# Kernel optimization log

Hardware: AMD Instinct MI355X
Metric: run time of the kernel (lower is better)

The kernel has to match this reference:

```python
import jax, jax.numpy as jnp
import numpy as np

DIM = 768
NUM_HEADS = 12
DIM_HEAD = 64
INNER = NUM_HEADS * DIM_HEAD  # 768
SCALE = DIM_HEAD ** -0.5


def setup_inputs() -> dict:
    key = jax.random.key(0)
    k1, k2, k3 = jax.random.split(key, 3)
    B, N = 8, 1024
    x = jax.random.normal(k1, (B, N, DIM), dtype=jnp.float32)
    # Linear(dim, 3*inner_dim, bias=False): weight shape (out, in) torch-style
    w_qkv = jax.random.normal(k2, (3 * INNER, DIM), dtype=jnp.float32) * (DIM ** -0.5)
    # proj: Linear(inner_dim, dim, bias=False)
    w_proj = jax.random.normal(k3, (DIM, INNER), dtype=jnp.float32) * (INNER ** -0.5)
    return {"x": x, "w_qkv": w_qkv, "w_proj": w_proj}


def reference(x, w_qkv, w_proj):
    B, N, C = x.shape
    H, dh = NUM_HEADS, DIM_HEAD
    # qkv projection: (B,N,C) @ (C, 3*inner) -> (B,N,3*inner)
    qkv = jnp.einsum('bnc,oc->bno', x, w_qkv)
    qkv = qkv.reshape(B, N, 3, H, dh).transpose(2, 0, 3, 1, 4)  # (3,B,H,N,dh)
    q, k, v = qkv[0], qkv[1], qkv[2]
    # attention scores (B,H,N,N)
    attn_scores = jnp.einsum('bhnd,bhmd->bhnm', q, k) * SCALE
    attn_probs = jax.nn.softmax(attn_scores, axis=-1)
    # attention output (B,H,N,dh) -> (B,N,inner)
    attn_out = jnp.einsum('bhnm,bhmd->bhnd', attn_probs, v)
    attn_out = attn_out.transpose(0, 2, 1, 3).reshape(B, N, H * dh)
    out = jnp.einsum('bni,oi->bno', attn_out, w_proj)
    return out
```

## Files before the change

kernel.cpp:

```cpp
#include <hip/hip_runtime.h>
#include <stdint.h>

typedef unsigned short u16;
typedef __attribute__((ext_vector_type(8))) short short8;
typedef __attribute__((ext_vector_type(4))) short short4v;
typedef __attribute__((ext_vector_type(4))) float f32x4;

#define LOG2E 1.44269504088896340736f

#define Bb 8
#define NSEQ 1024
#define DIMC 768
#define NH 12
#define DH 64
#define INNER 768
#define MTOT (Bb*NSEQ)
#define QKVN (3*INNER)
#define HEADS_TOT (Bb*NH)
#define QKV_PART ((size_t)Bb*NH*NSEQ*DH)

static __device__ inline u16 f2bf(float f) {
    uint32_t u = __builtin_bit_cast(uint32_t, f);
    uint32_t r = (u + 0x7fffu + ((u >> 16) & 1u)) >> 16;
    return (u16)r;
}

static __device__ __forceinline__ uint32_t pkbf(float f0, float f1) {
    uint32_t u0 = __builtin_bit_cast(uint32_t, f0) + 0x8000u;
    uint32_t u1 = __builtin_bit_cast(uint32_t, f1) + 0x8000u;
    return __builtin_amdgcn_perm(u1, u0, 0x07060302u);
}

#if __has_builtin(__builtin_amdgcn_mfma_f32_16x16x16bf16_1k)
static __device__ __forceinline__ f32x4 mfma16(short4v a, short4v b, f32x4 c) {
    return __builtin_amdgcn_mfma_f32_16x16x16bf16_1k(a, b, c, 0, 0, 0);
}
#else
static __device__ __forceinline__ f32x4 mfma16(short4v a, short4v b, f32x4 c) {
    asm volatile("v_mfma_f32_16x16x16_bf16 %0, %1, %2, %0\n\ts_nop 7\n\ts_nop 7"
                 : "+v"(c) : "v"(a), "v"(b));
    return c;
}
#endif

typedef __attribute__((address_space(1))) const void gas_void;
typedef __attribute__((address_space(3))) void las_void;
static __device__ __forceinline__ void async16(u16* lds, const u16* g) {
    __builtin_amdgcn_global_load_lds((gas_void*)(uintptr_t)g,
                                     (las_void*)(uintptr_t)lds, 16, 0, 0);
}

#define NX8  786432
#define NWQ8 221184
#define NWP8 73728
#define NCVT (NX8 + NWQ8 + NWP8)
__global__ __launch_bounds__(256) void cvt_all(const float* __restrict__ x,
                                               const float* __restrict__ wq,
                                               const float* __restrict__ wp,
                                               u16* __restrict__ xb,
                                               u16* __restrict__ wqb,
                                               u16* __restrict__ wpb) {
    int i = blockIdx.x * 256 + threadIdx.x;
    const float* s; u16* d; int j;
    if (i < NX8) { s = x; d = xb; j = i; }
    else if (i < NX8 + NWQ8) { s = wq; d = wqb; j = i - NX8; }
    else { s = wp; d = wpb; j = i - NX8 - NWQ8; }
    const float4* s4 = (const float4*)s;
    float4 a = s4[2 * j], b = s4[2 * j + 1];
    float v[8] = {a.x, a.y, a.z, a.w, b.x, b.y, b.z, b.w};
    u16 o[8];
#pragma unroll
    for (int t = 0; t < 8; t++) o[t] = f2bf(v[t]);
    ((uint4*)d)[j] = *(const uint4*)o;
}

#define BK 32
__global__ __launch_bounds__(512, 4) void gemm_qkv(const u16* __restrict__ A,
                                                   const u16* __restrict__ Bm,
                                                   u16* __restrict__ qkv) {
    __shared__ u16 As[128 * BK];
    __shared__ u16 Bs[256 * BK];
    const int tid = threadIdx.x;
    const int w = tid >> 6, lane = tid & 63, quad = lane >> 4, l16 = lane & 15;
    const int wr = w >> 2, wc = w & 3;
    const int m0 = blockIdx.y * 128;
    const int n0 = blockIdx.x * 256;
    const int K = DIMC;

    const int rl = lane >> 2, cc = lane & 3;
    const int ra = w * 16 + rl;
    const u16* agp = A + (size_t)(m0 + ra) * K + ((cc - ((ra >> 1) & 3)) & 3) * 8;
    u16* alp = As + (w * 16) * BK;
    const u16* bgp[2]; u16* blp[2];
#pragma unroll
    for (int j = 0; j < 2; j++) {
        int rb = w * 32 + j * 16 + rl;
        bgp[j] = Bm + (size_t)(n0 + rb) * K + ((cc - ((rb >> 1) & 3)) & 3) * 8;
        blp[j] = Bs + (w * 32 + j * 16) * BK;
    }

    const int swz = ((quad + ((l16 >> 1) & 3)) & 3) * 8;
    int aoff[4], boff[4];
#pragma unroll
    for (int t = 0; t < 4; t++) {
        aoff[t] = (wr * 64 + t * 16 + l16) * BK + swz;
        boff[t] = (wc * 64 + t * 16 + l16) * BK + swz;
    }

    f32x4 acc[4][4] = {};
    for (int kt = 0; kt < K; kt += BK) {
        __syncthreads();
        async16(alp, agp + kt);
        async16(blp[0], bgp[0] + kt);
        async16(blp[1], bgp[1] + kt);
        __syncthreads();
        short8 af[4], bf[4];
#pragma unroll
        for (int t = 0; t < 4; t++) af[t] = *(const short8*)(As + aoff[t]);
#pragma unroll
        for (int t = 0; t < 4; t++) bf[t] = *(const short8*)(Bs + boff[t]);
#pragma unroll
        for (int mt = 0; mt < 4; mt++)
#pragma unroll
            for (int nt = 0; nt < 4; nt++)
                acc[mt][nt] = __builtin_amdgcn_mfma_f32_16x16x32_bf16(af[mt], bf[nt],
                                                                      acc[mt][nt], 0, 0, 0);
    }

#pragma unroll
    for (int nt = 0; nt < 4; nt++) {
        int o = n0 + wc * 64 + nt * 16 + l16;
        int which = o / 768;
        int rem = o - which * 768;
        int h = rem >> 6, d = rem & 63;
        if (which == 2) {
            u16* vt = qkv + 2 * QKV_PART;
#pragma unroll
            for (int mt = 0; mt < 4; mt++) {
                int m = m0 + wr * 64 + mt * 16 + quad * 4;
                int bb = m >> 10, ns = m & 1023;
                alignas(8) u16 pk[4];
#pragma unroll
                for (int r = 0; r < 4; r++) pk[r] = f2bf(acc[mt][nt][r]);
                *(uint2*)(vt + ((size_t)(bb * NH + h) * DH + d) * NSEQ + ns) =
                    *(const uint2*)pk;
            }
        } else {
            float sc = (which == 0) ? (0.125f * LOG2E) : 1.0f;
#pragma unroll
            for (int mt = 0; mt < 4; mt++)
#pragma unroll
                for (int r = 0; r < 4; r++) {
                    int m = m0 + wr * 64 + mt * 16 + quad * 4 + r;
                    int bb = m >> 10, ns = m & 1023;
                    size_t idx = (size_t)which * QKV_PART +
                                 (((size_t)(bb * NH + h) * NSEQ + ns) << 6) + d;
                    qkv[idx] = f2bf(acc[mt][nt][r] * sc);
                }
        }
    }
}

__global__ __launch_bounds__(256) void gemm_proj(const u16* __restrict__ A,
                                                 const u16* __restrict__ Bm,
                                                 float* __restrict__ Co) {
    __shared__ u16 As[128 * BK];
    __shared__ u16 Bs[128 * BK];
    const int tid = threadIdx.x;
    const int w = tid >> 6, lane = tid & 63, quad = lane >> 4, l16 = lane & 15;
    const int wr = w >> 1, wc = w & 1;
    const int m0 = blockIdx.y * 128;
    const int n0 = blockIdx.x * 128;
    const int K = INNER, N = DIMC;

    const int rl = lane >> 2, cc = lane & 3;
    const u16* ag[2]; const u16* bg[2]; u16* al[2]; u16* bl[2];
#pragma unroll
    for (int j = 0; j < 2; j++) {
        int r = w * 32 + j * 16 + rl;
        int c = ((cc - ((r >> 1) & 3)) & 3) * 8;
        ag[j] = A + (size_t)(m0 + r) * K + c;
        bg[j] = Bm + (size_t)(n0 + r) * K + c;
        al[j] = As + (w * 32 + j * 16) * BK;
        bl[j] = Bs + (w * 32 + j * 16) * BK;
    }
    const int swz = ((quad + ((l16 >> 1) & 3)) & 3) * 8;
    int aoff[4], boff[4];
#pragma unroll
    for (int t = 0; t < 4; t++) {
        aoff[t] = (wr * 64 + t * 16 + l16) * BK + swz;
        boff[t] = (wc * 64 + t * 16 + l16) * BK + swz;
    }

    f32x4 acc[4][4] = {};
    for (int kt = 0; kt < K; kt += BK) {
        __syncthreads();
#pragma unroll
        for (int j = 0; j < 2; j++) {
            async16(al[j], ag[j] + kt);
            async16(bl[j], bg[j] + kt);
        }
        __syncthreads();
        short8 af[4], bf[4];
#pragma unroll
        for (int t = 0; t < 4; t++) af[t] = *(const short8*)(As + aoff[t]);
#pragma unroll
        for (int t = 0; t < 4; t++) bf[t] = *(const short8*)(Bs + boff[t]);
#pragma unroll
        for (int mt = 0; mt < 4; mt++)
#pragma unroll
            for (int nt = 0; nt < 4; nt++)
                acc[mt][nt] = __builtin_amdgcn_mfma_f32_16x16x32_bf16(af[mt], bf[nt],
                                                                      acc[mt][nt], 0, 0, 0);
    }
#pragma unroll
    for (int mt = 0; mt < 4; mt++)
#pragma unroll
        for (int nt = 0; nt < 4; nt++) {
            int o = n0 + wc * 64 + nt * 16 + l16;
#pragma unroll
            for (int r = 0; r < 4; r++) {
                int m = m0 + wr * 64 + mt * 16 + quad * 4 + r;
                Co[(size_t)m * N + o] = acc[mt][nt][r];
            }
        }
}

__global__ __launch_bounds__(256) void attn_kernel(const u16* __restrict__ qkv,
                                                   u16* __restrict__ attn) {
    __shared__ u16 Ks[64 * 64];
    __shared__ u16 Vs[64 * 64];

    const int tid = threadIdx.x;
    const int w = tid >> 6, lane = tid & 63, quad = lane >> 4, l16 = lane & 15;
    const int bh = blockIdx.y, qt = blockIdx.x;
    const size_t headoff = (size_t)bh * NSEQ * DH;
    const u16* Qp = qkv + headoff;
    const u16* Kp = qkv + QKV_PART + headoff;
    const u16* Vtp = qkv + 2 * QKV_PART + headoff;
    const int q0 = qt * 128 + w * 32;

    const int rl8 = lane >> 3, cc8 = lane & 7;
    const u16* kg[2]; const u16* vg[2]; u16* kl[2]; u16* vl[2];
#pragma unroll
    for (int j = 0; j < 2; j++) {
        int r = w * 16 + j * 8 + rl8;
        int c = ((cc8 - r) & 7) * 8;
        kg[j] = Kp + (size_t)r * DH + c;
        vg[j] = Vtp + (size_t)r * NSEQ + c;
        kl[j] = Ks + (w * 16 + j * 8) * 64;
        vl[j] = Vs + (w * 16 + j * 8) * 64;
    }

    const int sw0 = ((quad + l16) & 7) * 8;
    const int sw1 = ((quad + 4 + l16) & 7) * 8;

    short8 qf[2][2];
#pragma unroll
    for (int mf = 0; mf < 2; mf++) {
        qf[mf][0] = *(const short8*)(Qp + (size_t)(q0 + mf * 16 + l16) * DH + quad * 8);
        qf[mf][1] = *(const short8*)(Qp + (size_t)(q0 + mf * 16 + l16) * DH + 32 + quad * 8);
    }

    f32x4 oacc[2][4] = {};
    float lsum[2] = {0.f, 0.f};

    for (int kt = 0; kt < NSEQ; kt += 64) {
        __syncthreads();
#pragma unroll
        for (int j = 0; j < 2; j++) {
            async16(kl[j], kg[j] + (size_t)kt * DH);
            async16(vl[j], vg[j] + kt);
        }
        __syncthreads();

        short8 kf[4][2];
#pragma unroll
        for (int nt = 0; nt < 4; nt++) {
            const u16* kr = Ks + (nt * 16 + l16) * 64;
            kf[nt][0] = *(const short8*)(kr + sw0);
            kf[nt][1] = *(const short8*)(kr + sw1);
        }
        short4v vf[4][4];
#pragma unroll
        for (int nt2 = 0; nt2 < 4; nt2++) {
            int row = nt2 * 16 + l16;
#pragma unroll
            for (int c = 0; c < 4; c++) {
                int off = row * 64 + (((c * 2 + (quad >> 1) + row) & 7) << 3) + (quad & 1) * 4;
                vf[nt2][c] = *(const short4v*)(Vs + off);
            }
        }

#pragma unroll
        for (int mf = 0; mf < 2; mf++) {
            f32x4 st[4];
#pragma unroll
            for (int nt = 0; nt < 4; nt++) {
                f32x4 z = {};
                z = __builtin_amdgcn_mfma_f32_16x16x32_bf16(kf[nt][0], qf[mf][0], z, 0, 0, 0);
                z = __builtin_amdgcn_mfma_f32_16x16x32_bf16(kf[nt][1], qf[mf][1], z, 0, 0, 0);
                st[nt] = z;
            }
            short4v pf[4];
#pragma unroll
            for (int c = 0; c < 4; c++) {
                float p0 = __builtin_amdgcn_exp2f(st[c][0]);
                float p1 = __builtin_amdgcn_exp2f(st[c][1]);
                float p2 = __builtin_amdgcn_exp2f(st[c][2]);
                float p3 = __builtin_amdgcn_exp2f(st[c][3]);
                lsum[mf] += (p0 + p1) + (p2 + p3);
                uint2 u = {pkbf(p0, p1), pkbf(p2, p3)};
                pf[c] = __builtin_bit_cast(short4v, u);
            }
#pragma unroll
            for (int nt2 = 0; nt2 < 4; nt2++)
#pragma unroll
                for (int c = 0; c < 4; c++)
                    oacc[mf][nt2] = mfma16(vf[nt2][c], pf[c], oacc[mf][nt2]);
        }
    }

#pragma unroll
    for (int mf = 0; mf < 2; mf++) {
        float v = lsum[mf];
        v += __shfl_xor(v, 16);
        v += __shfl_xor(v, 32);
        lsum[mf] = 1.0f / v;
    }

    const int b = bh / NH, h = bh - (bh / NH) * NH;
#pragma unroll
    for (int mf = 0; mf < 2; mf++) {
        int q = q0 + mf * 16 + l16;
        float inv = lsum[mf];
#pragma unroll
        for (int nt2 = 0; nt2 < 4; nt2++) {
            uint2 u = {pkbf(oacc[mf][nt2][0] * inv, oacc[mf][nt2][1] * inv),
                       pkbf(oacc[mf][nt2][2] * inv, oacc[mf][nt2][3] * inv)};
            int d = nt2 * 16 + quad * 4;
            *(uint2*)(attn + ((size_t)(b * NSEQ + q)) * INNER + h * DH + d) = u;
        }
    }
}

extern "C" void kernel_launch(void* const* d_in, const int* in_sizes, int n_in,
                              void* d_out, int out_size, void* d_ws, size_t ws_size,
                              hipStream_t stream) {
    const float* x = (const float*)d_in[0];
    const float* w_qkv = (const float*)d_in[1];
    const float* w_proj = (const float*)d_in[2];
    float* out = (float*)d_out;

    u16* xb = (u16*)d_ws;
    u16* wqkvb = xb + 6291456;
    u16* wprojb = wqkvb + 1769472;
    u16* qkvb = wprojb + 589824;
    u16* attnb = qkvb + 18874368;

    cvt_all<<<NCVT / 256, 256, 0, stream>>>(x, w_qkv, w_proj, xb, wqkvb, wprojb);

    dim3 g1(QKVN / 256, MTOT / 128);
    gemm_qkv<<<g1, 512, 0, stream>>>(xb, wqkvb, qkvb);

    dim3 g2(NSEQ / 128, HEADS_TOT);
    attn_kernel<<<g2, 256, 0, stream>>>(qkvb, attnb);

    dim3 g3(INNER / 128, MTOT / 128);
    gemm_proj<<<g3, 256, 0, stream>>>(attnb, wprojb, out);
}
```

Baseline: 207.1 us.

## Double K-tile depth in GEMMs and attention, add XCD-aware block remapping

Both GEMMs move from a 32-wide to a 64-wide K tile with an 8-chunk XOR swizzle, which halves the number of barrier pairs per output tile. Attention now stages 128 keys per iteration instead of 64 and processes them in two halves. Block indices are remapped so that blocks sharing A rows land on the same XCD, and the attention grid is transposed so heads vary fastest. The intent is to cut synchronisation overhead and improve L2 locality, at the cost of double the shared memory per block, which may reduce occupancy.

```diff
diff --git a/kernel.cpp b/kernel.cpp
--- a/kernel.cpp
+++ b/kernel.cpp
@@ -74,7 +74,7 @@
     ((uint4*)d)[j] = *(const uint4*)o;
 }
 
-#define BK 32
+#define BK 64
 __global__ __launch_bounds__(512, 4) void gemm_qkv(const u16* __restrict__ A,
                                                    const u16* __restrict__ Bm,
                                                    u16* __restrict__ qkv) {
@@ -83,48 +83,59 @@
     const int tid = threadIdx.x;
     const int w = tid >> 6, lane = tid & 63, quad = lane >> 4, l16 = lane & 15;
     const int wr = w >> 2, wc = w & 3;
-    const int m0 = blockIdx.y * 128;
-    const int n0 = blockIdx.x * 256;
+    const int bid = blockIdx.x + 9 * blockIdx.y;
+    const int xcd = bid & 7, slot = bid >> 3;
+    const int m0 = (xcd + 8 * (slot / 9)) * 128;
+    const int n0 = (slot % 9) * 256;
     const int K = DIMC;
 
-    const int rl = lane >> 2, cc = lane & 3;
-    const int ra = w * 16 + rl;
-    const u16* agp = A + (size_t)(m0 + ra) * K + ((cc - ((ra >> 1) & 3)) & 3) * 8;
-    u16* alp = As + (w * 16) * BK;
-    const u16* bgp[2]; u16* blp[2];
+    const int rl8 = lane >> 3, cc8 = lane & 7;
+    const u16* agp[2]; int asl[2];
 #pragma unroll
     for (int j = 0; j < 2; j++) {
-        int rb = w * 32 + j * 16 + rl;
-        bgp[j] = Bm + (size_t)(n0 + rb) * K + ((cc - ((rb >> 1) & 3)) & 3) * 8;
-        blp[j] = Bs + (w * 32 + j * 16) * BK;
-    }
-
-    const int swz = ((quad + ((l16 >> 1) & 3)) & 3) * 8;
-    int aoff[4], boff[4];
+        int r = w * 16 + j * 8 + rl8;
+        agp[j] = A + (size_t)(m0 + r) * K + ((cc8 - r) & 7) * 8;
+        asl[j] = (w * 16 + j * 8) * BK;
+    }
+    const u16* bgp[4]; int bsl[4];
+#pragma unroll
+    for (int j = 0; j < 4; j++) {
+        int r = w * 32 + j * 8 + rl8;
+        bgp[j] = Bm + (size_t)(n0 + r) * K + ((cc8 - r) & 7) * 8;
+        bsl[j] = (w * 32 + j * 8) * BK;
+    }
+
+    int abase[4], bbase[4], sw[2];
 #pragma unroll
     for (int t = 0; t < 4; t++) {
-        aoff[t] = (wr * 64 + t * 16 + l16) * BK + swz;
-        boff[t] = (wc * 64 + t * 16 + l16) * BK + swz;
-    }
+        abase[t] = (wr * 64 + t * 16 + l16) * BK;
+        bbase[t] = (wc * 64 + t * 16 + l16) * BK;
+    }
+#pragma unroll
+    for (int kc = 0; kc < 2; kc++) sw[kc] = ((quad + 4 * kc + l16) & 7) * 8;
 
     f32x4 acc[4][4] = {};
     for (int kt = 0; kt < K; kt += BK) {
         __syncthreads();
-        async16(alp, agp + kt);
-        async16(blp[0], bgp[0] + kt);
-        async16(blp[1], bgp[1] + kt);
-        __syncthreads();
-        short8 af[4], bf[4];
-#pragma unroll
-        for (int t = 0; t < 4; t++) af[t] = *(const short8*)(As + aoff[t]);
-#pragma unroll
-        for (int t = 0; t < 4; t++) bf[t] = *(const short8*)(Bs + boff[t]);
-#pragma unroll
-        for (int mt = 0; mt < 4; mt++)
-#pragma unroll
-            for (int nt = 0; nt < 4; nt++)
-                acc[mt][nt] = __builtin_amdgcn_mfma_f32_16x16x32_bf16(af[mt], bf[nt],
-                                                                      acc[mt][nt], 0, 0, 0);
+#pragma unroll
+        for (int j = 0; j < 2; j++) async16(As + asl[j], agp[j] + kt);
+#pragma unroll
+        for (int j = 0; j < 4; j++) async16(Bs + bsl[j], bgp[j] + kt);
+        __syncthreads();
+#pragma unroll
+        for (int kc = 0; kc < 2; kc++) {
+            short8 af[4], bf[4];
+#pragma unroll
+            for (int t = 0; t < 4; t++) af[t] = *(const short8*)(As + abase[t] + sw[kc]);
+#pragma unroll
+            for (int t = 0; t < 4; t++) bf[t] = *(const short8*)(Bs + bbase[t] + sw[kc]);
+#pragma unroll
+            for (int mt = 0; mt < 4; mt++)
+#pragma unroll
+                for (int nt = 0; nt < 4; nt++)
+                    acc[mt][nt] = __builtin_amdgcn_mfma_f32_16x16x32_bf16(af[mt], bf[nt],
+                                                                          acc[mt][nt], 0, 0, 0);
+        }
     }
 
 #pragma unroll
@@ -169,49 +180,55 @@
     const int tid = threadIdx.x;
     const int w = tid >> 6, lane = tid & 63, quad = lane >> 4, l16 = lane & 15;
     const int wr = w >> 1, wc = w & 1;
-    const int m0 = blockIdx.y * 128;
-    const int n0 = blockIdx.x * 128;
+    const int bid = blockIdx.x + 6 * blockIdx.y;
+    const int xcd = bid & 7, slot = bid >> 3;
+    const int m0 = (xcd + 8 * (slot / 6)) * 128;
+    const int n0 = (slot % 6) * 128;
     const int K = INNER, N = DIMC;
 
-    const int rl = lane >> 2, cc = lane & 3;
-    const u16* ag[2]; const u16* bg[2]; u16* al[2]; u16* bl[2];
-#pragma unroll
-    for (int j = 0; j < 2; j++) {
-        int r = w * 32 + j * 16 + rl;
-        int c = ((cc - ((r >> 1) & 3)) & 3) * 8;
-        ag[j] = A + (size_t)(m0 + r) * K + c;
-        bg[j] = Bm + (size_t)(n0 + r) * K + c;
-        al[j] = As + (w * 32 + j * 16) * BK;
-        bl[j] = Bs + (w * 32 + j * 16) * BK;
-    }
-    const int swz = ((quad + ((l16 >> 1) & 3)) & 3) * 8;
-    int aoff[4], boff[4];
+    const int rl8 = lane >> 3, cc8 = lane & 7;
+    const u16* agp[4]; const u16* bgp[4]; int asl[4];
+#pragma unroll
+    for (int j = 0; j < 4; j++) {
+        int r = w * 32 + j * 8 + rl8;
+        int c = ((cc8 - r) & 7) * 8;
+        agp[j] = A + (size_t)(m0 + r) * K + c;
+        bgp[j] = Bm + (size_t)(n0 + r) * K + c;
+        asl[j] = (w * 32 + j * 8) * BK;
+    }
+
+    int abase[4], bbase[4], sw[2];
 #pragma unroll
     for (int t = 0; t < 4; t++) {
-        aoff[t] = (wr * 64 + t * 16 + l16) * BK + swz;
-        boff[t] = (wc * 64 + t * 16 + l16) * BK + swz;
-    }
+        abase[t] = (wr * 64 + t * 16 + l16) * BK;
+        bbase[t] = (wc * 64 + t * 16 + l16) * BK;
+    }
+#pragma unroll
+    for (int kc = 0; kc < 2; kc++) sw[kc] = ((quad + 4 * kc + l16) & 7) * 8;
 
     f32x4 acc[4][4] = {};
     for (int kt = 0; kt < K; kt += BK) {
         __syncthreads();
 #pragma unroll
-        for (int j = 0; j < 2; j++) {
-            async16(al[j], ag[j] + kt);
-            async16(bl[j], bg[j] + kt);
-        }
-        __syncthreads();
-        short8 af[4], bf[4];
-#pragma unroll
-        for (int t = 0; t < 4; t++) af[t] = *(const short8*)(As + aoff[t]);
-#pragma unroll
-        for (int t = 0; t < 4; t++) bf[t] = *(const short8*)(Bs + boff[t]);
-#pragma unroll
-        for (int mt = 0; mt < 4; mt++)
-#pragma unroll
-            for (int nt = 0; nt < 4; nt++)
-                acc[mt][nt] = __builtin_amdgcn_mfma_f32_16x16x32_bf16(af[mt], bf[nt],
-                                                                      acc[mt][nt], 0, 0, 0);
+        for (int j = 0; j < 4; j++) {
+            async16(As + asl[j], agp[j] + kt);
+            async16(Bs + asl[j], bgp[j] + kt);
+        }
+        __syncthreads();
+#pragma unroll
+        for (int kc = 0; kc < 2; kc++) {
+            short8 af[4], bf[4];
+#pragma unroll
+            for (int t = 0; t < 4; t++) af[t] = *(const short8*)(As + abase[t] + sw[kc]);
+#pragma unroll
+            for (int t = 0; t < 4; t++) bf[t] = *(const short8*)(Bs + bbase[t] + sw[kc]);
+#pragma unroll
+            for (int mt = 0; mt < 4; mt++)
+#pragma unroll
+                for (int nt = 0; nt < 4; nt++)
+                    acc[mt][nt] = __builtin_amdgcn_mfma_f32_16x16x32_bf16(af[mt], bf[nt],
+                                                                          acc[mt][nt], 0, 0, 0);
+        }
     }
 #pragma unroll
     for (int mt = 0; mt < 4; mt++)
@@ -228,12 +245,12 @@
 
 __global__ __launch_bounds__(256) void attn_kernel(const u16* __restrict__ qkv,
                                                    u16* __restrict__ attn) {
-    __shared__ u16 Ks[64 * 64];
-    __shared__ u16 Vs[64 * 64];
+    __shared__ u16 Ks[128 * 64];
+    __shared__ u16 Vs[64 * 128];
 
     const int tid = threadIdx.x;
     const int w = tid >> 6, lane = tid & 63, quad = lane >> 4, l16 = lane & 15;
-    const int bh = blockIdx.y, qt = blockIdx.x;
+    const int bh = blockIdx.x, qt = blockIdx.y;
     const size_t headoff = (size_t)bh * NSEQ * DH;
     const u16* Qp = qkv + headoff;
     const u16* Kp = qkv + QKV_PART + headoff;
@@ -241,15 +258,20 @@
     const int q0 = qt * 128 + w * 32;
 
     const int rl8 = lane >> 3, cc8 = lane & 7;
-    const u16* kg[2]; const u16* vg[2]; u16* kl[2]; u16* vl[2];
-#pragma unroll
-    for (int j = 0; j < 2; j++) {
-        int r = w * 16 + j * 8 + rl8;
-        int c = ((cc8 - r) & 7) * 8;
-        kg[j] = Kp + (size_t)r * DH + c;
-        vg[j] = Vtp + (size_t)r * NSEQ + c;
-        kl[j] = Ks + (w * 16 + j * 8) * 64;
-        vl[j] = Vs + (w * 16 + j * 8) * 64;
+    const u16* kg[4]; int ksl[4];
+#pragma unroll
+    for (int j = 0; j < 4; j++) {
+        int r = w * 32 + j * 8 + rl8;
+        kg[j] = Kp + (size_t)r * DH + ((cc8 - r) & 7) * 8;
+        ksl[j] = (w * 32 + j * 8) * 64;
+    }
+    const int cc16 = lane & 15;
+    const u16* vg[4]; int vsl[4];
+#pragma unroll
+    for (int j = 0; j < 4; j++) {
+        int r = w * 16 + j * 4 + quad;
+        vg[j] = Vtp + (size_t)r * NSEQ + ((cc16 - r) & 15) * 8;
+        vsl[j] = (w * 16 + j * 4) * 128;
     }
 
     const int sw0 = ((quad + l16) & 7) * 8;
@@ -265,59 +287,63 @@
     f32x4 oacc[2][4] = {};
     float lsum[2] = {0.f, 0.f};
 
-    for (int kt = 0; kt < NSEQ; kt += 64) {
-        __syncthreads();
-#pragma unroll
-        for (int j = 0; j < 2; j++) {
-            async16(kl[j], kg[j] + (size_t)kt * DH);
-            async16(vl[j], vg[j] + kt);
-        }
-        __syncthreads();
-
-        short8 kf[4][2];
-#pragma unroll
-        for (int nt = 0; nt < 4; nt++) {
-            const u16* kr = Ks + (nt * 16 + l16) * 64;
-            kf[nt][0] = *(const short8*)(kr + sw0);
-            kf[nt][1] = *(const short8*)(kr + sw1);
-        }
-        short4v vf[4][4];
-#pragma unroll
-        for (int nt2 = 0; nt2 < 4; nt2++) {
-            int row = nt2 * 16 + l16;
-#pragma unroll
-            for (int c = 0; c < 4; c++) {
-                int off = row * 64 + (((c * 2 + (quad >> 1) + row) & 7) << 3) + (quad & 1) * 4;
-                vf[nt2][c] = *(const short4v*)(Vs + off);
-            }
-        }
-
-#pragma unroll
-        for (int mf = 0; mf < 2; mf++) {
-            f32x4 st[4];
+    for (int kt = 0; kt < NSEQ; kt += 128) {
+        __syncthreads();
+#pragma unroll
+        for (int j = 0; j < 4; j++) {
+            async16(Ks + ksl[j], kg[j] + (size_t)kt * DH);
+            async16(Vs + vsl[j], vg[j] + kt);
+        }
+        __syncthreads();
+
+#pragma unroll
+        for (int half = 0; half < 2; half++) {
+            short8 kf[4][2];
 #pragma unroll
             for (int nt = 0; nt < 4; nt++) {
-                f32x4 z = {};
-                z = __builtin_amdgcn_mfma_f32_16x16x32_bf16(kf[nt][0], qf[mf][0], z, 0, 0, 0);
-                z = __builtin_amdgcn_mfma_f32_16x16x32_bf16(kf[nt][1], qf[mf][1], z, 0, 0, 0);
-                st[nt] = z;
-            }
-            short4v pf[4];
-#pragma unroll
-            for (int c = 0; c < 4; c++) {
-                float p0 = __builtin_amdgcn_exp2f(st[c][0]);
-                float p1 = __builtin_amdgcn_exp2f(st[c][1]);
-                float p2 = __builtin_amdgcn_exp2f(st[c][2]);
-                float p3 = __builtin_amdgcn_exp2f(st[c][3]);
-                lsum[mf] += (p0 + p1) + (p2 + p3);
-                uint2 u = {pkbf(p0, p1), pkbf(p2, p3)};
-                pf[c] = __builtin_bit_cast(short4v, u);
-            }
-#pragma unroll
-            for (int nt2 = 0; nt2 < 4; nt2++)
-#pragma unroll
-                for (int c = 0; c < 4; c++)
-                    oacc[mf][nt2] = mfma16(vf[nt2][c], pf[c], oacc[mf][nt2]);
+                const u16* kr = Ks + (half * 64 + nt * 16 + l16) * 64;
+                kf[nt][0] = *(const short8*)(kr + sw0);
+                kf[nt][1] = *(const short8*)(kr + sw1);
+            }
+            short4v vf[4][4];
+#pragma unroll
+            for (int nt2 = 0; nt2 < 4; nt2++) {
+                int row = nt2 * 16 + l16;
+#pragma unroll
+                for (int c = 0; c < 4; c++) {
+                    int chunk = half * 8 + c * 2 + (quad >> 1);
+                    int off = row * 128 + (((chunk + row) & 15) << 3) + (quad & 1) * 4;
+                    vf[nt2][c] = *(const short4v*)(Vs + off);
+                }
+            }
+
+#pragma unroll
+            for (int mf = 0; mf < 2; mf++) {
+                f32x4 st[4];
+#pragma unroll
+                for (int nt = 0; nt < 4; nt++) {
+                    f32x4 z = {};
+                    z = __builtin_amdgcn_mfma_f32_16x16x32_bf16(kf[nt][0], qf[mf][0], z, 0, 0, 0);
+                    z = __builtin_amdgcn_mfma_f32_16x16x32_bf16(kf[nt][1], qf[mf][1], z, 0, 0, 0);
+                    st[nt] = z;
+                }
+                short4v pf[4];
+#pragma unroll
+                for (int c = 0; c < 4; c++) {
+                    float p0 = __builtin_amdgcn_exp2f(st[c][0]);
+                    float p1 = __builtin_amdgcn_exp2f(st[c][1]);
+                    float p2 = __builtin_amdgcn_exp2f(st[c][2]);
+                    float p3 = __builtin_amdgcn_exp2f(st[c][3]);
+                    lsum[mf] += (p0 + p1) + (p2 + p3);
+                    uint2 u = {pkbf(p0, p1), pkbf(p2, p3)};
+                    pf[c] = __builtin_bit_cast(short4v, u);
+                }
+#pragma unroll
+                for (int nt2 = 0; nt2 < 4; nt2++)
+#pragma unroll
+                    for (int c = 0; c < 4; c++)
+                        oacc[mf][nt2] = mfma16(vf[nt2][c], pf[c], oacc[mf][nt2]);
+            }
         }
     }
 
@@ -363,7 +389,7 @@
     dim3 g1(QKVN / 256, MTOT / 128);
     gemm_qkv<<<g1, 512, 0, stream>>>(xb, wqkvb, qkvb);
 
-    dim3 g2(NSEQ / 128, HEADS_TOT);
+    dim3 g2(HEADS_TOT, NSEQ / 128);
     attn_kernel<<<g2, 256, 0, stream>>>(qkvb, attnb);
 
     dim3 g3(INNER / 128, MTOT / 128);
```

After: 209.5 us. Within noise of the previous version (+1.2%).

## Register-prefetch pipelining in GEMMs and attention, unify GEMM kernels with BK=64

Applied to the files above, without the earlier changes.

Replaces the async global-to-LDS loads with register prefetching. The next tile's global loads are issued right after the current tile is stored to LDS, so they overlap with the MFMA work. Both GEMMs become one templated 128x128 kernel with BK=64, which halves the number of K-loop barriers, and the QKV GEMM switches from 128x256 tiles with 512 threads to 128x128 with 256 threads. Attention blocks are remapped so heads vary fastest across blockIdx.x. The cost is more registers for the prefetch buffers, with possible occupancy loss, plus an extra VGPR-to-LDS store step.

```diff
diff --git a/kernel.cpp b/kernel.cpp
--- a/kernel.cpp
+++ b/kernel.cpp
@@ -42,13 +42,6 @@
     return c;
 }
 #endif
-
-typedef __attribute__((address_space(1))) const void gas_void;
-typedef __attribute__((address_space(3))) void las_void;
-static __device__ __forceinline__ void async16(u16* lds, const u16* g) {
-    __builtin_amdgcn_global_load_lds((gas_void*)(uintptr_t)g,
-                                     (las_void*)(uintptr_t)lds, 16, 0, 0);
-}
 
 #define NX8  786432
 #define NWQ8 221184
@@ -74,96 +67,13 @@
     ((uint4*)d)[j] = *(const uint4*)o;
 }
 
-#define BK 32
-__global__ __launch_bounds__(512, 4) void gemm_qkv(const u16* __restrict__ A,
-                                                   const u16* __restrict__ Bm,
-                                                   u16* __restrict__ qkv) {
-    __shared__ u16 As[128 * BK];
-    __shared__ u16 Bs[256 * BK];
-    const int tid = threadIdx.x;
-    const int w = tid >> 6, lane = tid & 63, quad = lane >> 4, l16 = lane & 15;
-    const int wr = w >> 2, wc = w & 3;
-    const int m0 = blockIdx.y * 128;
-    const int n0 = blockIdx.x * 256;
-    const int K = DIMC;
-
-    const int rl = lane >> 2, cc = lane & 3;
-    const int ra = w * 16 + rl;
-    const u16* agp = A + (size_t)(m0 + ra) * K + ((cc - ((ra >> 1) & 3)) & 3) * 8;
-    u16* alp = As + (w * 16) * BK;
-    const u16* bgp[2]; u16* blp[2];
-#pragma unroll
-    for (int j = 0; j < 2; j++) {
-        int rb = w * 32 + j * 16 + rl;
-        bgp[j] = Bm + (size_t)(n0 + rb) * K + ((cc - ((rb >> 1) & 3)) & 3) * 8;
-        blp[j] = Bs + (w * 32 + j * 16) * BK;
-    }
-
-    const int swz = ((quad + ((l16 >> 1) & 3)) & 3) * 8;
-    int aoff[4], boff[4];
-#pragma unroll
-    for (int t = 0; t < 4; t++) {
-        aoff[t] = (wr * 64 + t * 16 + l16) * BK + swz;
-        boff[t] = (wc * 64 + t * 16 + l16) * BK + swz;
-    }
-
-    f32x4 acc[4][4] = {};
-    for (int kt = 0; kt < K; kt += BK) {
-        __syncthreads();
-        async16(alp, agp + kt);
-        async16(blp[0], bgp[0] + kt);
-        async16(blp[1], bgp[1] + kt);
-        __syncthreads();
-        short8 af[4], bf[4];
-#pragma unroll
-        for (int t = 0; t < 4; t++) af[t] = *(const short8*)(As + aoff[t]);
-#pragma unroll
-        for (int t = 0; t < 4; t++) bf[t] = *(const short8*)(Bs + boff[t]);
-#pragma unroll
-        for (int mt = 0; mt < 4; mt++)
-#pragma unroll
-            for (int nt = 0; nt < 4; nt++)
-                acc[mt][nt] = __builtin_amdgcn_mfma_f32_16x16x32_bf16(af[mt], bf[nt],
-                                                                      acc[mt][nt], 0, 0, 0);
-    }
-
-#pragma unroll
-    for (int nt = 0; nt < 4; nt++) {
-        int o = n0 + wc * 64 + nt * 16 + l16;
-        int which = o / 768;
-        int rem = o - which * 768;
-        int h = rem >> 6, d = rem & 63;
-        if (which == 2) {
-            u16* vt = qkv + 2 * QKV_PART;
-#pragma unroll
-            for (int mt = 0; mt < 4; mt++) {
-                int m = m0 + wr * 64 + mt * 16 + quad * 4;
-                int bb = m >> 10, ns = m & 1023;
-                alignas(8) u16 pk[4];
-#pragma unroll
-                for (int r = 0; r < 4; r++) pk[r] = f2bf(acc[mt][nt][r]);
-                *(uint2*)(vt + ((size_t)(bb * NH + h) * DH + d) * NSEQ + ns) =
-                    *(const uint2*)pk;
-            }
-        } else {
-            float sc = (which == 0) ? (0.125f * LOG2E) : 1.0f;
-#pragma unroll
-            for (int mt = 0; mt < 4; mt++)
-#pragma unroll
-                for (int r = 0; r < 4; r++) {
-                    int m = m0 + wr * 64 + mt * 16 + quad * 4 + r;
-                    int bb = m >> 10, ns = m & 1023;
-                    size_t idx = (size_t)which * QKV_PART +
-                                 (((size_t)(bb * NH + h) * NSEQ + ns) << 6) + d;
-                    qkv[idx] = f2bf(acc[mt][nt][r] * sc);
-                }
-        }
-    }
-}
-
-__global__ __launch_bounds__(256) void gemm_proj(const u16* __restrict__ A,
-                                                 const u16* __restrict__ Bm,
-                                                 float* __restrict__ Co) {
+#define BK 64
+
+template <int MODE>
+__global__ __launch_bounds__(256) void gemm_bt(const u16* __restrict__ A,
+                                               const u16* __restrict__ Bm,
+                                               void* __restrict__ Cout,
+                                               int K, int N) {
     __shared__ u16 As[128 * BK];
     __shared__ u16 Bs[128 * BK];
     const int tid = threadIdx.x;
@@ -171,59 +81,113 @@
     const int wr = w >> 1, wc = w & 1;
     const int m0 = blockIdx.y * 128;
     const int n0 = blockIdx.x * 128;
-    const int K = INNER, N = DIMC;
-
-    const int rl = lane >> 2, cc = lane & 3;
-    const u16* ag[2]; const u16* bg[2]; u16* al[2]; u16* bl[2];
-#pragma unroll
-    for (int j = 0; j < 2; j++) {
-        int r = w * 32 + j * 16 + rl;
-        int c = ((cc - ((r >> 1) & 3)) & 3) * 8;
-        ag[j] = A + (size_t)(m0 + r) * K + c;
-        bg[j] = Bm + (size_t)(n0 + r) * K + c;
-        al[j] = As + (w * 32 + j * 16) * BK;
-        bl[j] = Bs + (w * 32 + j * 16) * BK;
-    }
-    const int swz = ((quad + ((l16 >> 1) & 3)) & 3) * 8;
-    int aoff[4], boff[4];
+
+    const int sr = tid >> 3, sc = tid & 7;
+    const u16* agp[4]; const u16* bgp[4]; int lsl[4];
+#pragma unroll
+    for (int j = 0; j < 4; j++) {
+        int r = j * 32 + sr;
+        agp[j] = A + (size_t)(m0 + r) * K + sc * 8;
+        bgp[j] = Bm + (size_t)(n0 + r) * K + sc * 8;
+        lsl[j] = r * BK + ((sc + r) & 7) * 8;
+    }
+
+    int abase[4], bbase[4], sw[2];
 #pragma unroll
     for (int t = 0; t < 4; t++) {
-        aoff[t] = (wr * 64 + t * 16 + l16) * BK + swz;
-        boff[t] = (wc * 64 + t * 16 + l16) * BK + swz;
+        abase[t] = (wr * 64 + t * 16 + l16) * BK;
+        bbase[t] = (wc * 64 + t * 16 + l16) * BK;
+    }
+#pragma unroll
+    for (int kc = 0; kc < 2; kc++) sw[kc] = ((quad + 4 * kc + l16) & 7) * 8;
+
+    uint4 apre[4], bpre[4];
+#pragma unroll
+    for (int j = 0; j < 4; j++) {
+        apre[j] = *(const uint4*)(agp[j]);
+        bpre[j] = *(const uint4*)(bgp[j]);
     }
 
     f32x4 acc[4][4] = {};
-    for (int kt = 0; kt < K; kt += BK) {
+    const int NIT = K / BK;
+    for (int it = 0; it < NIT; ++it) {
         __syncthreads();
 #pragma unroll
-        for (int j = 0; j < 2; j++) {
-            async16(al[j], ag[j] + kt);
-            async16(bl[j], bg[j] + kt);
+        for (int j = 0; j < 4; j++) {
+            *(uint4*)(As + lsl[j]) = apre[j];
+            *(uint4*)(Bs + lsl[j]) = bpre[j];
+        }
+        int ktn = (it + 1 < NIT) ? (it + 1) * BK : 0;
+#pragma unroll
+        for (int j = 0; j < 4; j++) {
+            apre[j] = *(const uint4*)(agp[j] + ktn);
+            bpre[j] = *(const uint4*)(bgp[j] + ktn);
         }
         __syncthreads();
-        short8 af[4], bf[4];
-#pragma unroll
-        for (int t = 0; t < 4; t++) af[t] = *(const short8*)(As + aoff[t]);
-#pragma unroll
-        for (int t = 0; t < 4; t++) bf[t] = *(const short8*)(Bs + boff[t]);
-#pragma unroll
-        for (int mt = 0; mt < 4; mt++)
-#pragma unroll
-            for (int nt = 0; nt < 4; nt++)
-                acc[mt][nt] = __builtin_amdgcn_mfma_f32_16x16x32_bf16(af[mt], bf[nt],
-                                                                      acc[mt][nt], 0, 0, 0);
-    }
-#pragma unroll
-    for (int mt = 0; mt < 4; mt++)
+#pragma unroll
+        for (int kc = 0; kc < 2; kc++) {
+            short8 af[4], bf[4];
+#pragma unroll
+            for (int t = 0; t < 4; t++) af[t] = *(const short8*)(As + abase[t] + sw[kc]);
+#pragma unroll
+            for (int t = 0; t < 4; t++) bf[t] = *(const short8*)(Bs + bbase[t] + sw[kc]);
+#pragma unroll
+            for (int mt = 0; mt < 4; mt++)
+#pragma unroll
+                for (int nt = 0; nt < 4; nt++)
+                    acc[mt][nt] = __builtin_amdgcn_mfma_f32_16x16x32_bf16(af[mt], bf[nt],
+                                                                          acc[mt][nt], 0, 0, 0);
+        }
+    }
+
+    if (MODE == 0) {
+        u16* qkv = (u16*)Cout;
 #pragma unroll
         for (int nt = 0; nt < 4; nt++) {
             int o = n0 + wc * 64 + nt * 16 + l16;
-#pragma unroll
-            for (int r = 0; r < 4; r++) {
-                int m = m0 + wr * 64 + mt * 16 + quad * 4 + r;
-                Co[(size_t)m * N + o] = acc[mt][nt][r];
-            }
-        }
+            int which = o / 768;
+            int rem = o - which * 768;
+            int h = rem >> 6, d = rem & 63;
+            if (which == 2) {
+                u16* vt = qkv + 2 * QKV_PART;
+#pragma unroll
+                for (int mt = 0; mt < 4; mt++) {
+                    int m = m0 + wr * 64 + mt * 16 + quad * 4;
+                    int bb = m >> 10, ns = m & 1023;
+                    alignas(8) u16 pk[4];
+#pragma unroll
+                    for (int r = 0; r < 4; r++) pk[r] = f2bf(acc[mt][nt][r]);
+                    *(uint2*)(vt + ((size_t)(bb * NH + h) * DH + d) * NSEQ + ns) =
+                        *(const uint2*)pk;
+                }
+            } else {
+                float sc2 = (which == 0) ? (0.125f * LOG2E) : 1.0f;
+#pragma unroll
+                for (int mt = 0; mt < 4; mt++)
+#pragma unroll
+                    for (int r = 0; r < 4; r++) {
+                        int m = m0 + wr * 64 + mt * 16 + quad * 4 + r;
+                        int bb = m >> 10, ns = m & 1023;
+                        size_t idx = (size_t)which * QKV_PART +
+                                     (((size_t)(bb * NH + h) * NSEQ + ns) << 6) + d;
+                        qkv[idx] = f2bf(acc[mt][nt][r] * sc2);
+                    }
+            }
+        }
+    } else {
+        float* Co = (float*)Cout;
+#pragma unroll
+        for (int mt = 0; mt < 4; mt++)
+#pragma unroll
+            for (int nt = 0; nt < 4; nt++) {
+                int o = n0 + wc * 64 + nt * 16 + l16;
+#pragma unroll
+                for (int r = 0; r < 4; r++) {
+                    int m = m0 + wr * 64 + mt * 16 + quad * 4 + r;
+                    Co[(size_t)m * N + o] = acc[mt][nt][r];
+                }
+            }
+    }
 }
 
 __global__ __launch_bounds__(256) void attn_kernel(const u16* __restrict__ qkv,
@@ -233,23 +197,21 @@
 
     const int tid = threadIdx.x;
     const int w = tid >> 6, lane = tid & 63, quad = lane >> 4, l16 = lane & 15;
-    const int bh = blockIdx.y, qt = blockIdx.x;
+    const int bh = blockIdx.x, qt = blockIdx.y;
     const size_t headoff = (size_t)bh * NSEQ * DH;
     const u16* Qp = qkv + headoff;
     const u16* Kp = qkv + QKV_PART + headoff;
     const u16* Vtp = qkv + 2 * QKV_PART + headoff;
     const int q0 = qt * 128 + w * 32;
 
-    const int rl8 = lane >> 3, cc8 = lane & 7;
-    const u16* kg[2]; const u16* vg[2]; u16* kl[2]; u16* vl[2];
+    const int sr = tid >> 3, sc = tid & 7;
+    const u16* kg[2]; const u16* vg[2]; int lsl[2];
 #pragma unroll
     for (int j = 0; j < 2; j++) {
-        int r = w * 16 + j * 8 + rl8;
-        int c = ((cc8 - r) & 7) * 8;
-        kg[j] = Kp + (size_t)r * DH + c;
-        vg[j] = Vtp + (size_t)r * NSEQ + c;
-        kl[j] = Ks + (w * 16 + j * 8) * 64;
-        vl[j] = Vs + (w * 16 + j * 8) * 64;
+        int r = j * 32 + sr;
+        kg[j] = Kp + (size_t)r * DH + sc * 8;
+        vg[j] = Vtp + (size_t)r * NSEQ + sc * 8;
+        lsl[j] = r * 64 + ((sc + r) & 7) * 8;
     }
 
     const int sw0 = ((quad + l16) & 7) * 8;
@@ -262,15 +224,29 @@
         qf[mf][1] = *(const short8*)(Qp + (size_t)(q0 + mf * 16 + l16) * DH + 32 + quad * 8);
     }
 
+    uint4 kpre[2], vpre[2];
+#pragma unroll
+    for (int j = 0; j < 2; j++) {
+        kpre[j] = *(const uint4*)(kg[j]);
+        vpre[j] = *(const uint4*)(vg[j]);
+    }
+
     f32x4 oacc[2][4] = {};
     float lsum[2] = {0.f, 0.f};
 
-    for (int kt = 0; kt < NSEQ; kt += 64) {
+    const int NIT = NSEQ / 64;
+    for (int it = 0; it < NIT; ++it) {
         __syncthreads();
 #pragma unroll
         for (int j = 0; j < 2; j++) {
-            async16(kl[j], kg[j] + (size_t)kt * DH);
-            async16(vl[j], vg[j] + kt);
+            *(uint4*)(Ks + lsl[j]) = kpre[j];
+            *(uint4*)(Vs + lsl[j]) = vpre[j];
+        }
+        int ktn = (it + 1 < NIT) ? (it + 1) * 64 : 0;
+#pragma unroll
+        for (int j = 0; j < 2; j++) {
+            kpre[j] = *(const uint4*)(kg[j] + (size_t)ktn * DH);
+            vpre[j] = *(const uint4*)(vg[j] + ktn);
         }
         __syncthreads();
 
@@ -360,12 +336,12 @@
 
     cvt_all<<<NCVT / 256, 256, 0, stream>>>(x, w_qkv, w_proj, xb, wqkvb, wprojb);
 
-    dim3 g1(QKVN / 256, MTOT / 128);
-    gemm_qkv<<<g1, 512, 0, stream>>>(xb, wqkvb, qkvb);
-
-    dim3 g2(NSEQ / 128, HEADS_TOT);
+    dim3 g1(QKVN / 128, MTOT / 128);
+    gemm_bt<0><<<g1, 256, 0, stream>>>(xb, wqkvb, qkvb, DIMC, QKVN);
+
+    dim3 g2(HEADS_TOT, NSEQ / 128);
     attn_kernel<<<g2, 256, 0, stream>>>(qkvb, attnb);
 
     dim3 g3(INNER / 128, MTOT / 128);
-    gemm_proj<<<g3, 256, 0, stream>>>(attnb, wprojb, out);
-}
+    gemm_bt<1><<<g3, 256, 0, stream>>>(attnb, wprojb, out, INNER, DIMC);
+}
```

After: 365.4 us. +76.5%, slower.
